# Performance work log

Hardware: AMD Instinct MI355X
Metric: run time of the kernel (lower is better)

## Reference

```python
import jax, jax.numpy as jnp
import numpy as np

DIM_MODEL = 1024
NUM_HEADS = 16
DIM_K = DIM_MODEL // NUM_HEADS
B, S = 4, 2048


def setup_inputs() -> dict:
    key = jax.random.key(0)
    ks = jax.random.split(key, 11)
    std = 1.0 / np.sqrt(DIM_MODEL)  # kaiming_normal fan_in, gain sqrt(2)/sqrt(fan_in); use simple scale
    kaiming = np.sqrt(2.0 / DIM_MODEL)
    return {
        "query": jax.random.normal(ks[0], (B, S, DIM_MODEL), dtype=jnp.float32),
        "key": jax.random.normal(ks[1], (B, S, DIM_MODEL), dtype=jnp.float32),
        "value": jax.random.normal(ks[2], (B, S, DIM_MODEL), dtype=jnp.float32),
        "W_q": jax.random.normal(ks[3], (DIM_MODEL, DIM_MODEL), dtype=jnp.float32) * kaiming,
        "b_q": jnp.zeros((DIM_MODEL,), dtype=jnp.float32),
        "W_k": jax.random.normal(ks[4], (DIM_MODEL, DIM_MODEL), dtype=jnp.float32) * kaiming,
        "b_k": jnp.zeros((DIM_MODEL,), dtype=jnp.float32),
        "W_v": jax.random.normal(ks[5], (DIM_MODEL, DIM_MODEL), dtype=jnp.float32) * kaiming,
        "b_v": jnp.zeros((DIM_MODEL,), dtype=jnp.float32),
        "W_o": jax.random.normal(ks[6], (DIM_MODEL, DIM_MODEL), dtype=jnp.float32) * kaiming,
        "b_o": jnp.zeros((DIM_MODEL,), dtype=jnp.float32),
    }


def _split_heads(x):
    b, s, _ = x.shape
    return x.reshape(b, s, NUM_HEADS, DIM_K).transpose(0, 2, 1, 3)  # [B,H,S,Dk]


def reference(query, key, value, W_q, b_q, W_k, b_k, W_v, b_v, W_o, b_o):
    # torch Linear: y = x @ W.T + b; dropout p=0.0 -> identity
    q = _split_heads(query @ W_q.T + b_q)
    k = _split_heads(key @ W_k.T + b_k)
    v = _split_heads(value @ W_v.T + b_v)
    scale = 1.0 / np.sqrt(DIM_K)
    scores = jnp.einsum("bhqd,bhkd->bhqk", q, k) * scale  # [B,H,S,S]
    probs = jax.nn.softmax(scores, axis=-1)
    attn = jnp.einsum("bhqk,bhkd->bhqd", probs, v)
    out = attn.transpose(0, 2, 1, 3).reshape(query.shape[0], query.shape[1], DIM_MODEL)
    return out @ W_o.T + b_o
```

## Files before the change

### kernel.cpp

```cpp
#include <hip/hip_runtime.h>
#include <stdint.h>

typedef __bf16 bf16x8 __attribute__((ext_vector_type(8)));
typedef __bf16 bf16x4 __attribute__((ext_vector_type(4)));
typedef float f32x4 __attribute__((ext_vector_type(4)));

static __device__ __forceinline__ unsigned short f2bf(float f) {
  unsigned u = __builtin_bit_cast(unsigned, f);
  u += 0x7fffu + ((u >> 16) & 1u);
  return (unsigned short)(u >> 16);
}

static __device__ __forceinline__ unsigned short bfu(float x) {
  __bf16 b = (__bf16)x;
  return __builtin_bit_cast(unsigned short, b);
}

#if __has_builtin(__builtin_amdgcn_exp2f)
#define EXP2(x) __builtin_amdgcn_exp2f(x)
#else
#define EXP2(x) __expf(0.69314718055994531f * (x))
#endif

static __device__ __forceinline__ void gload_lds16(const void* g, void* l) {
  __builtin_amdgcn_global_load_lds(
      (const __attribute__((address_space(1))) unsigned int*)(uintptr_t)g,
      (__attribute__((address_space(3))) unsigned int*)(uintptr_t)l, 16, 0, 0);
}

#define BIGU 2097152
#define WU   262144
__global__ __launch_bounds__(256) void cvt_all(const float* __restrict__ q,  const float* __restrict__ k,
                                               const float* __restrict__ v,  const float* __restrict__ wq,
                                               const float* __restrict__ wk, const float* __restrict__ wv,
                                               const float* __restrict__ wo, ushort4* __restrict__ dst) {
  int u = blockIdx.x * 256 + threadIdx.x;
  const float4* src;
  if (u < BIGU)            src = (const float4*)q + u;
  else if (u < 2 * BIGU)   src = (const float4*)k + (u - BIGU);
  else if (u < 3 * BIGU)   src = (const float4*)v + (u - 2 * BIGU);
  else {
    int r = u - 3 * BIGU;
    if (r < WU)            src = (const float4*)wq + r;
    else if (r < 2 * WU)   src = (const float4*)wk + (r - WU);
    else if (r < 3 * WU)   src = (const float4*)wv + (r - 2 * WU);
    else                   src = (const float4*)wo + (r - 3 * WU);
  }
  float4 f = *src;
  ushort4 o;
  o.x = f2bf(f.x); o.y = f2bf(f.y); o.z = f2bf(f.z); o.w = f2bf(f.w);
  dst[u] = o;
}

#define GM 8192
#define GN 1024
#define GK 1024

template <bool OUTF32, bool TRIPLE>
__global__ __launch_bounds__(256, 2) void gemm_bt(const unsigned short* __restrict__ A0,
                                                  const unsigned short* __restrict__ W0,
                                                  const float* __restrict__ bias0,
                                                  const float* __restrict__ bias1,
                                                  const float* __restrict__ bias2,
                                                  void* __restrict__ Cout) {
  __shared__ unsigned short As[2][128 * 64];
  __shared__ unsigned short Bs[2][128 * 64];
  const int z = TRIPLE ? blockIdx.z : 0;
  const unsigned short* A  = A0 + (size_t)z * ((size_t)GM * GK);
  const unsigned short* Bw = W0 + (size_t)z * ((size_t)GN * GK);
  const float* bias = TRIPLE ? (z == 0 ? bias0 : (z == 1 ? bias1 : bias2)) : bias0;

  const int tid = threadIdx.x;
  const int w = tid >> 6;
  const int lane = tid & 63;
  const int lq = lane & 15;
  const int g = lane >> 4;
  const int bm = blockIdx.y * 128;
  const int bn = blockIdx.x * 128;
  const int srow = lane >> 3;
  const int schunk = (lane & 7) ^ srow;
  const int wrow = (w >> 1) * 64;
  const int wcol = (w & 1) * 64;

  f32x4 acc[4][4] = {};

#define STAGE(ktv, bufv)                                                                   \
  do {                                                                                     \
    _Pragma("unroll") for (int j = 0; j < 4; ++j) {                                        \
      const int r0 = w * 32 + j * 8;                                                       \
      gload_lds16(A  + (size_t)(bm + r0 + srow) * GK + (ktv) * 64 + schunk * 8,            \
                  &As[bufv][r0 * 64]);                                                     \
      gload_lds16(Bw + (size_t)(bn + r0 + srow) * GK + (ktv) * 64 + schunk * 8,            \
                  &Bs[bufv][r0 * 64]);                                                     \
    }                                                                                      \
  } while (0)

  STAGE(0, 0);
  __syncthreads();

  for (int kt = 0; kt < GK / 64; ++kt) {
    const int cur = kt & 1;
    if (kt < GK / 64 - 1) STAGE(kt + 1, cur ^ 1);

#pragma unroll
    for (int kk = 0; kk < 2; ++kk) {
      bf16x8 af[4], bfv[4];
#pragma unroll
      for (int mt = 0; mt < 4; ++mt) {
        int m = wrow + mt * 16 + lq;
        af[mt] = *(const bf16x8*)&As[cur][m * 64 + ((kk * 32 + g * 8) ^ ((m & 7) << 3))];
      }
#pragma unroll
      for (int nt = 0; nt < 4; ++nt) {
        int n = wcol + nt * 16 + lq;
        bfv[nt] = *(const bf16x8*)&Bs[cur][n * 64 + ((kk * 32 + g * 8) ^ ((n & 7) << 3))];
      }
#pragma unroll
      for (int mt = 0; mt < 4; ++mt)
#pragma unroll
        for (int nt = 0; nt < 4; ++nt)
          acc[mt][nt] = __builtin_amdgcn_mfma_f32_16x16x32_bf16(af[mt], bfv[nt], acc[mt][nt], 0, 0, 0);
    }
    __syncthreads();
  }
#undef STAGE

  float bvs[4];
#pragma unroll
  for (int nt = 0; nt < 4; ++nt) bvs[nt] = bias[bn + wcol + nt * 16 + lq];

#pragma unroll
  for (int mt = 0; mt < 4; ++mt) {
#pragma unroll
    for (int nt = 0; nt < 4; ++nt) {
#pragma unroll
      for (int r = 0; r < 4; ++r) {
        int m = bm + wrow + mt * 16 + g * 4 + r;
        int n = bn + wcol + nt * 16 + lq;
        float v = acc[mt][nt][r] + bvs[nt];
        if (OUTF32) ((float*)Cout)[(size_t)m * GN + n] = v;
        else ((unsigned short*)Cout)[(size_t)z * ((size_t)GM * GN) + (size_t)m * GN + n] = f2bf(v);
      }
    }
  }
}

#define TRRD(dst, off) \
  asm volatile("ds_read_b64_tr_b16 %0, %1 offset:" off \
               : "=v"(dst) \
               : "v"((const __attribute__((address_space(3))) unsigned short*)(uintptr_t)vb))

__global__ __launch_bounds__(256, 3) void attn_fwd(const unsigned short* __restrict__ Qp,
                                                   const unsigned short* __restrict__ Kp,
                                                   const unsigned short* __restrict__ Vp,
                                                   unsigned short* __restrict__ Op) {
  __shared__ unsigned short Ks[2][4096];
  __shared__ unsigned short Vs[2][4096];
  __shared__ unsigned short Pl[8][1024];
  const int tid = threadIdx.x;
  const int w = tid >> 6;
  const int lane = tid & 63;
  const int lq = lane & 15;
  const int g = lane >> 4;
  const int qt = blockIdx.x;
  const int bh = blockIdx.y;
  const int b = bh >> 4;
  const int h = bh & 15;
  const size_t rowbase = (size_t)b * 2048;
  const int hcol = h * 64;

  const int c0 = w * 2, c1 = w * 2 + 1;
  const int srow = lane >> 3;
  const int schunk = (lane & 7) ^ srow;
  const int vkeyl = (lane >> 5) * 4 + ((lane >> 1) & 3);
  const int vd0   = ((lane >> 3) & 3) * 16 + (lane & 1) * 8;

  const unsigned short* kq = Kp + rowbase * 1024 + hcol;
  const unsigned short* vq = Vp + rowbase * 1024 + hcol;

  bf16x8 qf[2][2];
#pragma unroll
  for (int qh = 0; qh < 2; ++qh) {
    const int qrow = qt * 128 + w * 32 + qh * 16 + lq;
#pragma unroll
    for (int kk = 0; kk < 2; ++kk)
      qf[qh][kk] = *(const bf16x8*)&Qp[(rowbase + qrow) * 1024 + hcol + kk * 32 + g * 8];
  }

  const float ks2 = 0.125f * 1.44269504088896f;
  float m0 = -1e30f, m1 = -1e30f, l0 = 0.f, l1 = 0.f;
  f32x4 oa[2][4] = {};
  unsigned short* Pw0 = Pl[w * 2];
  unsigned short* Pw1 = Pl[w * 2 + 1];
  const int pxor = (lq & 7) << 3;
  const int kxor = pxor;

  {
    gload_lds16(kq + (size_t)(c0 * 8 + srow) * 1024 + schunk * 8, &Ks[0][c0 * 512]);
    gload_lds16(kq + (size_t)(c1 * 8 + srow) * 1024 + schunk * 8, &Ks[0][c1 * 512]);
    gload_lds16(vq + (size_t)(c0 * 8 + vkeyl) * 1024 + vd0, &Vs[0][c0 * 512]);
    gload_lds16(vq + (size_t)(c1 * 8 + vkeyl) * 1024 + vd0, &Vs[0][c1 * 512]);
  }
  __syncthreads();

  for (int j = 0; j < 32; ++j) {
    const int cur = j & 1;
    if (j < 31) {
      const size_t so = (size_t)(j + 1) * 64 * 1024;
      gload_lds16(kq + so + (size_t)(c0 * 8 + srow) * 1024 + schunk * 8, &Ks[cur ^ 1][c0 * 512]);
      gload_lds16(kq + so + (size_t)(c1 * 8 + srow) * 1024 + schunk * 8, &Ks[cur ^ 1][c1 * 512]);
      gload_lds16(vq + so + (size_t)(c0 * 8 + vkeyl) * 1024 + vd0, &Vs[cur ^ 1][c0 * 512]);
      gload_lds16(vq + so + (size_t)(c1 * 8 + vkeyl) * 1024 + vd0, &Vs[cur ^ 1][c1 * 512]);
    }

    f32x4 cc[2][4];
#pragma unroll
    for (int qh = 0; qh < 2; ++qh)
#pragma unroll
      for (int t = 0; t < 4; ++t) cc[qh][t] = (f32x4){0.f, 0.f, 0.f, 0.f};
#pragma unroll
    for (int t = 0; t < 4; ++t) {
      const int rb = (t * 16 + lq) * 64;
#pragma unroll
      for (int kk = 0; kk < 2; ++kk) {
        bf16x8 kf = *(const bf16x8*)&Ks[cur][rb + ((kk * 32 + g * 8) ^ kxor)];
        cc[0][t] = __builtin_amdgcn_mfma_f32_16x16x32_bf16(kf, qf[0][kk], cc[0][t], 0, 0, 0);
        cc[1][t] = __builtin_amdgcn_mfma_f32_16x16x32_bf16(kf, qf[1][kk], cc[1][t], 0, 0, 0);
      }
    }

    float t0 = cc[0][0][0], t1 = cc[1][0][0];
#pragma unroll
    for (int t = 0; t < 4; ++t)
#pragma unroll
      for (int r = 0; r < 4; ++r) {
        t0 = fmaxf(t0, cc[0][t][r]);
        t1 = fmaxf(t1, cc[1][t][r]);
      }
    t0 = fmaxf(t0, __shfl_xor(t0, 16)); t0 = fmaxf(t0, __shfl_xor(t0, 32));
    t1 = fmaxf(t1, __shfl_xor(t1, 16)); t1 = fmaxf(t1, __shfl_xor(t1, 32));

    const int defer = (t0 - m0 <= 64.f) && (t1 - m1 <= 64.f);
    if (!__all(defer)) {
      float n0 = fmaxf(m0, t0), n1 = fmaxf(m1, t1);
      float cr0 = EXP2(ks2 * (m0 - n0)), cr1 = EXP2(ks2 * (m1 - n1));
      l0 *= cr0; l1 *= cr1;
#pragma unroll
      for (int dt = 0; dt < 4; ++dt) { oa[0][dt] *= cr0; oa[1][dt] *= cr1; }
      m0 = n0; m1 = n1;
    }
    const float mk0 = m0 * ks2, mk1 = m1 * ks2;
    float ps0 = 0.f, ps1 = 0.f;
#pragma unroll
    for (int t = 0; t < 4; ++t) {
      float a0 = EXP2(__builtin_fmaf(cc[0][t][0], ks2, -mk0));
      float a1 = EXP2(__builtin_fmaf(cc[0][t][1], ks2, -mk0));
      float a2 = EXP2(__builtin_fmaf(cc[0][t][2], ks2, -mk0));
      float a3 = EXP2(__builtin_fmaf(cc[0][t][3], ks2, -mk0));
      ps0 += (a0 + a1) + (a2 + a3);
      ushort4 pk0; pk0.x = bfu(a0); pk0.y = bfu(a1); pk0.z = bfu(a2); pk0.w = bfu(a3);
      *(ushort4*)&Pw0[lq * 64 + ((t * 16 + g * 4) ^ pxor)] = pk0;
      float b0 = EXP2(__builtin_fmaf(cc[1][t][0], ks2, -mk1));
      float b1 = EXP2(__builtin_fmaf(cc[1][t][1], ks2, -mk1));
      float b2 = EXP2(__builtin_fmaf(cc[1][t][2], ks2, -mk1));
      float b3 = EXP2(__builtin_fmaf(cc[1][t][3], ks2, -mk1));
      ps1 += (b0 + b1) + (b2 + b3);
      ushort4 pk1; pk1.x = bfu(b0); pk1.y = bfu(b1); pk1.z = bfu(b2); pk1.w = bfu(b3);
      *(ushort4*)&Pw1[lq * 64 + ((t * 16 + g * 4) ^ pxor)] = pk1;
    }
    l0 += ps0; l1 += ps1;

    bf16x8 pf[2][2];
#pragma unroll
    for (int qh = 0; qh < 2; ++qh) {
      unsigned short* Pw = qh ? Pw1 : Pw0;
#pragma unroll
      for (int kk = 0; kk < 2; ++kk)
        pf[qh][kk] = *(const bf16x8*)&Pw[lq * 64 + ((kk * 32 + g * 8) ^ pxor)];
    }
    const unsigned short* vb =
        &Vs[cur][g * 512 + ((lane >> 2) & 3) * 16 + (lane & 3) * 4];
    bf16x4 T[16];
    TRRD(T[0],  "0");    TRRD(T[1],  "128");  TRRD(T[2],  "256");  TRRD(T[3],  "384");
    TRRD(T[4],  "512");  TRRD(T[5],  "640");  TRRD(T[6],  "768");  TRRD(T[7],  "896");
    TRRD(T[8],  "4096"); TRRD(T[9],  "4224"); TRRD(T[10], "4352"); TRRD(T[11], "4480");
    TRRD(T[12], "4608"); TRRD(T[13], "4736"); TRRD(T[14], "4864"); TRRD(T[15], "4992");
    asm volatile("s_waitcnt lgkmcnt(0)" ::: "memory");
    __builtin_amdgcn_sched_barrier(0);
#pragma unroll
    for (int kk = 0; kk < 2; ++kk) {
#pragma unroll
      for (int dt = 0; dt < 4; ++dt) {
        bf16x8 vf = __builtin_shufflevector(T[kk * 8 + dt], T[kk * 8 + 4 + dt],
                                            0, 1, 2, 3, 4, 5, 6, 7);
        oa[0][dt] = __builtin_amdgcn_mfma_f32_16x16x32_bf16(vf, pf[0][kk], oa[0][dt], 0, 0, 0);
        oa[1][dt] = __builtin_amdgcn_mfma_f32_16x16x32_bf16(vf, pf[1][kk], oa[1][dt], 0, 0, 0);
      }
    }
    __syncthreads();
  }

  l0 += __shfl_xor(l0, 16); l0 += __shfl_xor(l0, 32);
  l1 += __shfl_xor(l1, 16); l1 += __shfl_xor(l1, 32);
  float inv0 = 1.0f / l0, inv1 = 1.0f / l1;
#pragma unroll
  for (int qh = 0; qh < 2; ++qh) {
    const float inv = qh ? inv1 : inv0;
    const int qrow = qt * 128 + w * 32 + qh * 16 + lq;
#pragma unroll
    for (int dt = 0; dt < 4; ++dt) {
      ushort4 pk;
      pk.x = bfu(oa[qh][dt][0] * inv);
      pk.y = bfu(oa[qh][dt][1] * inv);
      pk.z = bfu(oa[qh][dt][2] * inv);
      pk.w = bfu(oa[qh][dt][3] * inv);
      *(ushort4*)&Op[(rowbase + qrow) * 1024 + hcol + dt * 16 + g * 4] = pk;
    }
  }
}

extern "C" void kernel_launch(void* const* d_in, const int* in_sizes, int n_in,
                              void* d_out, int out_size, void* d_ws, size_t ws_size,
                              hipStream_t stream) {
  const float* q  = (const float*)d_in[0];
  const float* k  = (const float*)d_in[1];
  const float* v  = (const float*)d_in[2];
  const float* Wq = (const float*)d_in[3];
  const float* bq = (const float*)d_in[4];
  const float* Wk = (const float*)d_in[5];
  const float* bk = (const float*)d_in[6];
  const float* Wv = (const float*)d_in[7];
  const float* bv = (const float*)d_in[8];
  const float* Wo = (const float*)d_in[9];
  const float* bo = (const float*)d_in[10];

  unsigned short* ws = (unsigned short*)d_ws;
  const size_t SZ  = (size_t)8192 * 1024;
  const size_t WSZ = (size_t)1024 * 1024;
  unsigned short* Xq  = ws;
  unsigned short* Wqb = Xq + 3 * SZ;
  unsigned short* Qp  = Wqb + 4 * WSZ;
  unsigned short* Kp  = Qp + SZ;
  unsigned short* Vp  = Kp + SZ;
  unsigned short* Wob = Wqb + 3 * WSZ;
  unsigned short* At  = Xq;

  cvt_all<<<(3 * BIGU + 4 * WU) / 256, 256, 0, stream>>>(q, k, v, Wq, Wk, Wv, Wo, (ushort4*)ws);

  gemm_bt<false, true><<<dim3(GN / 128, GM / 128, 3), 256, 0, stream>>>(Xq, Wqb, bq, bk, bv, Qp);

  attn_fwd<<<dim3(16, 64), 256, 0, stream>>>(Qp, Kp, Vp, At);

  gemm_bt<true, false><<<dim3(GN / 128, GM / 128, 1), 256, 0, stream>>>(At, Wob, bo, bo, bo, (float*)d_out);
}
```

Before: 353.8 us.

## Double query rows per attention block and raise MFMA wave priority

```diff
diff --git a/kernel.cpp b/kernel.cpp
--- a/kernel.cpp
+++ b/kernel.cpp
@@ -150,13 +150,13 @@
                : "=v"(dst) \
                : "v"((const __attribute__((address_space(3))) unsigned short*)(uintptr_t)vb))
 
-__global__ __launch_bounds__(256, 3) void attn_fwd(const unsigned short* __restrict__ Qp,
+__global__ __launch_bounds__(256, 2) void attn_fwd(const unsigned short* __restrict__ Qp,
                                                    const unsigned short* __restrict__ Kp,
                                                    const unsigned short* __restrict__ Vp,
                                                    unsigned short* __restrict__ Op) {
   __shared__ unsigned short Ks[2][4096];
   __shared__ unsigned short Vs[2][4096];
-  __shared__ unsigned short Pl[8][1024];
+  __shared__ unsigned short Pl[16][1024];
   const int tid = threadIdx.x;
   const int w = tid >> 6;
   const int lane = tid & 63;
@@ -178,29 +178,26 @@
   const unsigned short* kq = Kp + rowbase * 1024 + hcol;
   const unsigned short* vq = Vp + rowbase * 1024 + hcol;
 
-  bf16x8 qf[2][2];
-#pragma unroll
-  for (int qh = 0; qh < 2; ++qh) {
-    const int qrow = qt * 128 + w * 32 + qh * 16 + lq;
+  bf16x8 qf[4][2];
+#pragma unroll
+  for (int qh = 0; qh < 4; ++qh) {
+    const int qrow = qt * 256 + w * 64 + qh * 16 + lq;
 #pragma unroll
     for (int kk = 0; kk < 2; ++kk)
       qf[qh][kk] = *(const bf16x8*)&Qp[(rowbase + qrow) * 1024 + hcol + kk * 32 + g * 8];
   }
 
   const float ks2 = 0.125f * 1.44269504088896f;
-  float m0 = -1e30f, m1 = -1e30f, l0 = 0.f, l1 = 0.f;
-  f32x4 oa[2][4] = {};
-  unsigned short* Pw0 = Pl[w * 2];
-  unsigned short* Pw1 = Pl[w * 2 + 1];
+  float mr[4] = {-1e30f, -1e30f, -1e30f, -1e30f};
+  float lr[4] = {0.f, 0.f, 0.f, 0.f};
+  f32x4 oa[4][4] = {};
   const int pxor = (lq & 7) << 3;
   const int kxor = pxor;
 
-  {
-    gload_lds16(kq + (size_t)(c0 * 8 + srow) * 1024 + schunk * 8, &Ks[0][c0 * 512]);
-    gload_lds16(kq + (size_t)(c1 * 8 + srow) * 1024 + schunk * 8, &Ks[0][c1 * 512]);
-    gload_lds16(vq + (size_t)(c0 * 8 + vkeyl) * 1024 + vd0, &Vs[0][c0 * 512]);
-    gload_lds16(vq + (size_t)(c1 * 8 + vkeyl) * 1024 + vd0, &Vs[0][c1 * 512]);
-  }
+  gload_lds16(kq + (size_t)(c0 * 8 + srow) * 1024 + schunk * 8, &Ks[0][c0 * 512]);
+  gload_lds16(kq + (size_t)(c1 * 8 + srow) * 1024 + schunk * 8, &Ks[0][c1 * 512]);
+  gload_lds16(vq + (size_t)(c0 * 8 + vkeyl) * 1024 + vd0, &Vs[0][c0 * 512]);
+  gload_lds16(vq + (size_t)(c1 * 8 + vkeyl) * 1024 + vd0, &Vs[0][c1 * 512]);
   __syncthreads();
 
   for (int j = 0; j < 32; ++j) {
@@ -213,67 +210,74 @@
       gload_lds16(vq + so + (size_t)(c1 * 8 + vkeyl) * 1024 + vd0, &Vs[cur ^ 1][c1 * 512]);
     }
 
-    f32x4 cc[2][4];
-#pragma unroll
-    for (int qh = 0; qh < 2; ++qh)
+    f32x4 cc[4][4];
+#pragma unroll
+    for (int qh = 0; qh < 4; ++qh)
 #pragma unroll
       for (int t = 0; t < 4; ++t) cc[qh][t] = (f32x4){0.f, 0.f, 0.f, 0.f};
+    __builtin_amdgcn_s_setprio(1);
 #pragma unroll
     for (int t = 0; t < 4; ++t) {
       const int rb = (t * 16 + lq) * 64;
 #pragma unroll
       for (int kk = 0; kk < 2; ++kk) {
         bf16x8 kf = *(const bf16x8*)&Ks[cur][rb + ((kk * 32 + g * 8) ^ kxor)];
-        cc[0][t] = __builtin_amdgcn_mfma_f32_16x16x32_bf16(kf, qf[0][kk], cc[0][t], 0, 0, 0);
-        cc[1][t] = __builtin_amdgcn_mfma_f32_16x16x32_bf16(kf, qf[1][kk], cc[1][t], 0, 0, 0);
-      }
-    }
-
-    float t0 = cc[0][0][0], t1 = cc[1][0][0];
-#pragma unroll
-    for (int t = 0; t < 4; ++t)
-#pragma unroll
-      for (int r = 0; r < 4; ++r) {
-        t0 = fmaxf(t0, cc[0][t][r]);
-        t1 = fmaxf(t1, cc[1][t][r]);
-      }
-    t0 = fmaxf(t0, __shfl_xor(t0, 16)); t0 = fmaxf(t0, __shfl_xor(t0, 32));
-    t1 = fmaxf(t1, __shfl_xor(t1, 16)); t1 = fmaxf(t1, __shfl_xor(t1, 32));
-
-    const int defer = (t0 - m0 <= 64.f) && (t1 - m1 <= 64.f);
+#pragma unroll
+        for (int qh = 0; qh < 4; ++qh)
+          cc[qh][t] = __builtin_amdgcn_mfma_f32_16x16x32_bf16(kf, qf[qh][kk], cc[qh][t], 0, 0, 0);
+      }
+    }
+    __builtin_amdgcn_s_setprio(0);
+
+    float tm[4];
+#pragma unroll
+    for (int qh = 0; qh < 4; ++qh) {
+      float t0 = cc[qh][0][0];
+#pragma unroll
+      for (int t = 0; t < 4; ++t)
+#pragma unroll
+        for (int r = 0; r < 4; ++r) t0 = fmaxf(t0, cc[qh][t][r]);
+      t0 = fmaxf(t0, __shfl_xor(t0, 16));
+      t0 = fmaxf(t0, __shfl_xor(t0, 32));
+      tm[qh] = t0;
+    }
+    int defer = 1;
+#pragma unroll
+    for (int qh = 0; qh < 4; ++qh) defer &= (tm[qh] - mr[qh] <= 64.f);
     if (!__all(defer)) {
-      float n0 = fmaxf(m0, t0), n1 = fmaxf(m1, t1);
-      float cr0 = EXP2(ks2 * (m0 - n0)), cr1 = EXP2(ks2 * (m1 - n1));
-      l0 *= cr0; l1 *= cr1;
-#pragma unroll
-      for (int dt = 0; dt < 4; ++dt) { oa[0][dt] *= cr0; oa[1][dt] *= cr1; }
-      m0 = n0; m1 = n1;
-    }
-    const float mk0 = m0 * ks2, mk1 = m1 * ks2;
-    float ps0 = 0.f, ps1 = 0.f;
-#pragma unroll
-    for (int t = 0; t < 4; ++t) {
-      float a0 = EXP2(__builtin_fmaf(cc[0][t][0], ks2, -mk0));
-      float a1 = EXP2(__builtin_fmaf(cc[0][t][1], ks2, -mk0));
-      float a2 = EXP2(__builtin_fmaf(cc[0][t][2], ks2, -mk0));
-      float a3 = EXP2(__builtin_fmaf(cc[0][t][3], ks2, -mk0));
-      ps0 += (a0 + a1) + (a2 + a3);
-      ushort4 pk0; pk0.x = bfu(a0); pk0.y = bfu(a1); pk0.z = bfu(a2); pk0.w = bfu(a3);
-      *(ushort4*)&Pw0[lq * 64 + ((t * 16 + g * 4) ^ pxor)] = pk0;
-      float b0 = EXP2(__builtin_fmaf(cc[1][t][0], ks2, -mk1));
-      float b1 = EXP2(__builtin_fmaf(cc[1][t][1], ks2, -mk1));
-      float b2 = EXP2(__builtin_fmaf(cc[1][t][2], ks2, -mk1));
-      float b3 = EXP2(__builtin_fmaf(cc[1][t][3], ks2, -mk1));
-      ps1 += (b0 + b1) + (b2 + b3);
-      ushort4 pk1; pk1.x = bfu(b0); pk1.y = bfu(b1); pk1.z = bfu(b2); pk1.w = bfu(b3);
-      *(ushort4*)&Pw1[lq * 64 + ((t * 16 + g * 4) ^ pxor)] = pk1;
-    }
-    l0 += ps0; l1 += ps1;
-
-    bf16x8 pf[2][2];
-#pragma unroll
-    for (int qh = 0; qh < 2; ++qh) {
-      unsigned short* Pw = qh ? Pw1 : Pw0;
+#pragma unroll
+      for (int qh = 0; qh < 4; ++qh) {
+        float n = fmaxf(mr[qh], tm[qh]);
+        float cr = EXP2(ks2 * (mr[qh] - n));
+        lr[qh] *= cr;
+#pragma unroll
+        for (int dt = 0; dt < 4; ++dt) oa[qh][dt] *= cr;
+        mr[qh] = n;
+      }
+    }
+#pragma unroll
+    for (int qh = 0; qh < 4; ++qh) {
+      const float mk = mr[qh] * ks2;
+      float ps = 0.f;
+      unsigned short* Pw = Pl[w * 4 + qh];
+#pragma unroll
+      for (int t = 0; t < 4; ++t) {
+        float a0 = EXP2(__builtin_fmaf(cc[qh][t][0], ks2, -mk));
+        float a1 = EXP2(__builtin_fmaf(cc[qh][t][1], ks2, -mk));
+        float a2 = EXP2(__builtin_fmaf(cc[qh][t][2], ks2, -mk));
+        float a3 = EXP2(__builtin_fmaf(cc[qh][t][3], ks2, -mk));
+        ps += (a0 + a1) + (a2 + a3);
+        ushort4 pk;
+        pk.x = bfu(a0); pk.y = bfu(a1); pk.z = bfu(a2); pk.w = bfu(a3);
+        *(ushort4*)&Pw[lq * 64 + ((t * 16 + g * 4) ^ pxor)] = pk;
+      }
+      lr[qh] += ps;
+    }
+
+    bf16x8 pf[4][2];
+#pragma unroll
+    for (int qh = 0; qh < 4; ++qh) {
+      unsigned short* Pw = Pl[w * 4 + qh];
 #pragma unroll
       for (int kk = 0; kk < 2; ++kk)
         pf[qh][kk] = *(const bf16x8*)&Pw[lq * 64 + ((kk * 32 + g * 8) ^ pxor)];
@@ -287,26 +291,29 @@
     TRRD(T[12], "4608"); TRRD(T[13], "4736"); TRRD(T[14], "4864"); TRRD(T[15], "4992");
     asm volatile("s_waitcnt lgkmcnt(0)" ::: "memory");
     __builtin_amdgcn_sched_barrier(0);
+    __builtin_amdgcn_s_setprio(1);
 #pragma unroll
     for (int kk = 0; kk < 2; ++kk) {
 #pragma unroll
       for (int dt = 0; dt < 4; ++dt) {
         bf16x8 vf = __builtin_shufflevector(T[kk * 8 + dt], T[kk * 8 + 4 + dt],
                                             0, 1, 2, 3, 4, 5, 6, 7);
-        oa[0][dt] = __builtin_amdgcn_mfma_f32_16x16x32_bf16(vf, pf[0][kk], oa[0][dt], 0, 0, 0);
-        oa[1][dt] = __builtin_amdgcn_mfma_f32_16x16x32_bf16(vf, pf[1][kk], oa[1][dt], 0, 0, 0);
-      }
-    }
+#pragma unroll
+        for (int qh = 0; qh < 4; ++qh)
+          oa[qh][dt] = __builtin_amdgcn_mfma_f32_16x16x32_bf16(vf, pf[qh][kk], oa[qh][dt], 0, 0, 0);
+      }
+    }
+    __builtin_amdgcn_s_setprio(0);
     __syncthreads();
   }
 
-  l0 += __shfl_xor(l0, 16); l0 += __shfl_xor(l0, 32);
-  l1 += __shfl_xor(l1, 16); l1 += __shfl_xor(l1, 32);
-  float inv0 = 1.0f / l0, inv1 = 1.0f / l1;
-#pragma unroll
-  for (int qh = 0; qh < 2; ++qh) {
-    const float inv = qh ? inv1 : inv0;
-    const int qrow = qt * 128 + w * 32 + qh * 16 + lq;
+#pragma unroll
+  for (int qh = 0; qh < 4; ++qh) {
+    float l = lr[qh];
+    l += __shfl_xor(l, 16);
+    l += __shfl_xor(l, 32);
+    const float inv = 1.0f / l;
+    const int qrow = qt * 256 + w * 64 + qh * 16 + lq;
 #pragma unroll
     for (int dt = 0; dt < 4; ++dt) {
       ushort4 pk;
@@ -349,7 +356,7 @@
 
   gemm_bt<false, true><<<dim3(GN / 128, GM / 128, 3), 256, 0, stream>>>(Xq, Wqb, bq, bk, bv, Qp);
 
-  attn_fwd<<<dim3(16, 64), 256, 0, stream>>>(Qp, Kp, Vp, At);
+  attn_fwd<<<dim3(8, 64), 256, 0, stream>>>(Qp, Kp, Vp, At);
 
   gemm_bt<true, false><<<dim3(GN / 128, GM / 128, 1), 256, 0, stream>>>(At, Wob, bo, bo, bo, (float*)d_out);
 }
```

Result: faster. 341.5 us (-3.5%).

## Switch attention to 32x32x16 MFMA and keep P in registers via permlane swap

Applied to the files above, without the earlier changes.

```diff
diff --git a/kernel.cpp b/kernel.cpp
--- a/kernel.cpp
+++ b/kernel.cpp
@@ -4,6 +4,7 @@
 typedef __bf16 bf16x8 __attribute__((ext_vector_type(8)));
 typedef __bf16 bf16x4 __attribute__((ext_vector_type(4)));
 typedef float f32x4 __attribute__((ext_vector_type(4)));
+typedef float f32x16 __attribute__((ext_vector_type(16)));
 
 static __device__ __forceinline__ unsigned short f2bf(float f) {
   unsigned u = __builtin_bit_cast(unsigned, f);
@@ -14,6 +15,27 @@
 static __device__ __forceinline__ unsigned short bfu(float x) {
   __bf16 b = (__bf16)x;
   return __builtin_bit_cast(unsigned short, b);
+}
+
+static __device__ __forceinline__ unsigned cvtpk(float lo, float hi) {
+  unsigned r;
+  asm("v_cvt_pk_bf16_f32 %0, %1, %2" : "=v"(r) : "v"(lo), "v"(hi));
+  return r;
+}
+
+static __device__ __forceinline__ void plswap(unsigned a, unsigned b,
+                                              unsigned& x, unsigned& y) {
+#if __has_builtin(__builtin_amdgcn_permlane32_swap)
+  auto r = __builtin_amdgcn_permlane32_swap((int)a, (int)b, false, false);
+  x = (unsigned)r[0];
+  y = (unsigned)r[1];
+#else
+  unsigned ap = (unsigned)__shfl_xor((int)a, 32);
+  unsigned bp = (unsigned)__shfl_xor((int)b, 32);
+  const bool lo = (threadIdx.x & 32) == 0;
+  x = lo ? a : bp;
+  y = lo ? ap : b;
+#endif
 }
 
 #if __has_builtin(__builtin_amdgcn_exp2f)
@@ -150,18 +172,17 @@
                : "=v"(dst) \
                : "v"((const __attribute__((address_space(3))) unsigned short*)(uintptr_t)vb))
 
-__global__ __launch_bounds__(256, 3) void attn_fwd(const unsigned short* __restrict__ Qp,
+__global__ __launch_bounds__(256, 4) void attn_fwd(const unsigned short* __restrict__ Qp,
                                                    const unsigned short* __restrict__ Kp,
                                                    const unsigned short* __restrict__ Vp,
                                                    unsigned short* __restrict__ Op) {
   __shared__ unsigned short Ks[2][4096];
   __shared__ unsigned short Vs[2][4096];
-  __shared__ unsigned short Pl[8][1024];
   const int tid = threadIdx.x;
   const int w = tid >> 6;
   const int lane = tid & 63;
-  const int lq = lane & 15;
-  const int g = lane >> 4;
+  const int q32 = lane & 31;
+  const int l5 = lane >> 5;
   const int qt = blockIdx.x;
   const int bh = blockIdx.y;
   const int b = bh >> 4;
@@ -178,29 +199,27 @@
   const unsigned short* kq = Kp + rowbase * 1024 + hcol;
   const unsigned short* vq = Vp + rowbase * 1024 + hcol;
 
-  bf16x8 qf[2][2];
-#pragma unroll
-  for (int qh = 0; qh < 2; ++qh) {
-    const int qrow = qt * 128 + w * 32 + qh * 16 + lq;
-#pragma unroll
-    for (int kk = 0; kk < 2; ++kk)
-      qf[qh][kk] = *(const bf16x8*)&Qp[(rowbase + qrow) * 1024 + hcol + kk * 32 + g * 8];
-  }
+  const int qrow = qt * 128 + w * 32 + q32;
+  bf16x8 qf[4];
+#pragma unroll
+  for (int ks = 0; ks < 4; ++ks)
+    qf[ks] = *(const bf16x8*)&Qp[(rowbase + qrow) * 1024 + hcol + ks * 16 + l5 * 8];
 
   const float ks2 = 0.125f * 1.44269504088896f;
-  float m0 = -1e30f, m1 = -1e30f, l0 = 0.f, l1 = 0.f;
-  f32x4 oa[2][4] = {};
-  unsigned short* Pw0 = Pl[w * 2];
-  unsigned short* Pw1 = Pl[w * 2 + 1];
-  const int pxor = (lq & 7) << 3;
-  const int kxor = pxor;
-
-  {
-    gload_lds16(kq + (size_t)(c0 * 8 + srow) * 1024 + schunk * 8, &Ks[0][c0 * 512]);
-    gload_lds16(kq + (size_t)(c1 * 8 + srow) * 1024 + schunk * 8, &Ks[0][c1 * 512]);
-    gload_lds16(vq + (size_t)(c0 * 8 + vkeyl) * 1024 + vd0, &Vs[0][c0 * 512]);
-    gload_lds16(vq + (size_t)(c1 * 8 + vkeyl) * 1024 + vd0, &Vs[0][c1 * 512]);
-  }
+  float mreg = -1e30f, lsum = 0.f;
+  f32x16 oa[2] = {};
+
+  const int rbase = q32 * 64;
+  const int kxor = (lane & 7) << 3;
+  int coff[4];
+#pragma unroll
+  for (int ks = 0; ks < 4; ++ks) coff[ks] = (ks * 16 + l5 * 8) ^ kxor;
+  const int vboff = l5 * 512 + ((lane >> 4) & 1) * 64 + ((lane >> 2) & 3) * 16 + (lane & 3) * 4;
+
+  gload_lds16(kq + (size_t)(c0 * 8 + srow) * 1024 + schunk * 8, &Ks[0][c0 * 512]);
+  gload_lds16(kq + (size_t)(c1 * 8 + srow) * 1024 + schunk * 8, &Ks[0][c1 * 512]);
+  gload_lds16(vq + (size_t)(c0 * 8 + vkeyl) * 1024 + vd0, &Vs[0][c0 * 512]);
+  gload_lds16(vq + (size_t)(c1 * 8 + vkeyl) * 1024 + vd0, &Vs[0][c1 * 512]);
   __syncthreads();
 
   for (int j = 0; j < 32; ++j) {
@@ -213,108 +232,88 @@
       gload_lds16(vq + so + (size_t)(c1 * 8 + vkeyl) * 1024 + vd0, &Vs[cur ^ 1][c1 * 512]);
     }
 
-    f32x4 cc[2][4];
-#pragma unroll
-    for (int qh = 0; qh < 2; ++qh)
-#pragma unroll
-      for (int t = 0; t < 4; ++t) cc[qh][t] = (f32x4){0.f, 0.f, 0.f, 0.f};
-#pragma unroll
-    for (int t = 0; t < 4; ++t) {
-      const int rb = (t * 16 + lq) * 64;
-#pragma unroll
-      for (int kk = 0; kk < 2; ++kk) {
-        bf16x8 kf = *(const bf16x8*)&Ks[cur][rb + ((kk * 32 + g * 8) ^ kxor)];
-        cc[0][t] = __builtin_amdgcn_mfma_f32_16x16x32_bf16(kf, qf[0][kk], cc[0][t], 0, 0, 0);
-        cc[1][t] = __builtin_amdgcn_mfma_f32_16x16x32_bf16(kf, qf[1][kk], cc[1][t], 0, 0, 0);
-      }
-    }
-
-    float t0 = cc[0][0][0], t1 = cc[1][0][0];
-#pragma unroll
-    for (int t = 0; t < 4; ++t)
-#pragma unroll
-      for (int r = 0; r < 4; ++r) {
-        t0 = fmaxf(t0, cc[0][t][r]);
-        t1 = fmaxf(t1, cc[1][t][r]);
-      }
-    t0 = fmaxf(t0, __shfl_xor(t0, 16)); t0 = fmaxf(t0, __shfl_xor(t0, 32));
-    t1 = fmaxf(t1, __shfl_xor(t1, 16)); t1 = fmaxf(t1, __shfl_xor(t1, 32));
-
-    const int defer = (t0 - m0 <= 64.f) && (t1 - m1 <= 64.f);
-    if (!__all(defer)) {
-      float n0 = fmaxf(m0, t0), n1 = fmaxf(m1, t1);
-      float cr0 = EXP2(ks2 * (m0 - n0)), cr1 = EXP2(ks2 * (m1 - n1));
-      l0 *= cr0; l1 *= cr1;
-#pragma unroll
-      for (int dt = 0; dt < 4; ++dt) { oa[0][dt] *= cr0; oa[1][dt] *= cr1; }
-      m0 = n0; m1 = n1;
-    }
-    const float mk0 = m0 * ks2, mk1 = m1 * ks2;
-    float ps0 = 0.f, ps1 = 0.f;
-#pragma unroll
-    for (int t = 0; t < 4; ++t) {
-      float a0 = EXP2(__builtin_fmaf(cc[0][t][0], ks2, -mk0));
-      float a1 = EXP2(__builtin_fmaf(cc[0][t][1], ks2, -mk0));
-      float a2 = EXP2(__builtin_fmaf(cc[0][t][2], ks2, -mk0));
-      float a3 = EXP2(__builtin_fmaf(cc[0][t][3], ks2, -mk0));
-      ps0 += (a0 + a1) + (a2 + a3);
-      ushort4 pk0; pk0.x = bfu(a0); pk0.y = bfu(a1); pk0.z = bfu(a2); pk0.w = bfu(a3);
-      *(ushort4*)&Pw0[lq * 64 + ((t * 16 + g * 4) ^ pxor)] = pk0;
-      float b0 = EXP2(__builtin_fmaf(cc[1][t][0], ks2, -mk1));
-      float b1 = EXP2(__builtin_fmaf(cc[1][t][1], ks2, -mk1));
-      float b2 = EXP2(__builtin_fmaf(cc[1][t][2], ks2, -mk1));
-      float b3 = EXP2(__builtin_fmaf(cc[1][t][3], ks2, -mk1));
-      ps1 += (b0 + b1) + (b2 + b3);
-      ushort4 pk1; pk1.x = bfu(b0); pk1.y = bfu(b1); pk1.z = bfu(b2); pk1.w = bfu(b3);
-      *(ushort4*)&Pw1[lq * 64 + ((t * 16 + g * 4) ^ pxor)] = pk1;
-    }
-    l0 += ps0; l1 += ps1;
-
-    bf16x8 pf[2][2];
-#pragma unroll
-    for (int qh = 0; qh < 2; ++qh) {
-      unsigned short* Pw = qh ? Pw1 : Pw0;
-#pragma unroll
-      for (int kk = 0; kk < 2; ++kk)
-        pf[qh][kk] = *(const bf16x8*)&Pw[lq * 64 + ((kk * 32 + g * 8) ^ pxor)];
-    }
-    const unsigned short* vb =
-        &Vs[cur][g * 512 + ((lane >> 2) & 3) * 16 + (lane & 3) * 4];
-    bf16x4 T[16];
-    TRRD(T[0],  "0");    TRRD(T[1],  "128");  TRRD(T[2],  "256");  TRRD(T[3],  "384");
-    TRRD(T[4],  "512");  TRRD(T[5],  "640");  TRRD(T[6],  "768");  TRRD(T[7],  "896");
-    TRRD(T[8],  "4096"); TRRD(T[9],  "4224"); TRRD(T[10], "4352"); TRRD(T[11], "4480");
-    TRRD(T[12], "4608"); TRRD(T[13], "4736"); TRRD(T[14], "4864"); TRRD(T[15], "4992");
-    asm volatile("s_waitcnt lgkmcnt(0)" ::: "memory");
-    __builtin_amdgcn_sched_barrier(0);
-#pragma unroll
-    for (int kk = 0; kk < 2; ++kk) {
-#pragma unroll
-      for (int dt = 0; dt < 4; ++dt) {
-        bf16x8 vf = __builtin_shufflevector(T[kk * 8 + dt], T[kk * 8 + 4 + dt],
-                                            0, 1, 2, 3, 4, 5, 6, 7);
-        oa[0][dt] = __builtin_amdgcn_mfma_f32_16x16x32_bf16(vf, pf[0][kk], oa[0][dt], 0, 0, 0);
-        oa[1][dt] = __builtin_amdgcn_mfma_f32_16x16x32_bf16(vf, pf[1][kk], oa[1][dt], 0, 0, 0);
-      }
+#pragma unroll
+    for (int kt = 0; kt < 2; ++kt) {
+      f32x16 c = {};
+      __builtin_amdgcn_s_setprio(1);
+#pragma unroll
+      for (int ks = 0; ks < 4; ++ks) {
+        bf16x8 kf = *(const bf16x8*)&Ks[cur][kt * 2048 + rbase + coff[ks]];
+        c = __builtin_amdgcn_mfma_f32_32x32x16_bf16(kf, qf[ks], c, 0, 0, 0);
+      }
+      __builtin_amdgcn_s_setprio(0);
+
+      const unsigned short* vb = &Vs[cur][kt * 2048 + vboff];
+      bf16x4 T[8];
+      TRRD(T[0], "0");    TRRD(T[1], "512");
+      TRRD(T[2], "256");  TRRD(T[3], "768");
+      TRRD(T[4], "2048"); TRRD(T[5], "2560");
+      TRRD(T[6], "2304"); TRRD(T[7], "2816");
+
+      float a0 = fmaxf(c[0], c[1]),   a1 = fmaxf(c[2], c[3]);
+      float a2 = fmaxf(c[4], c[5]),   a3 = fmaxf(c[6], c[7]);
+      float a4 = fmaxf(c[8], c[9]),   a5 = fmaxf(c[10], c[11]);
+      float a6 = fmaxf(c[12], c[13]), a7 = fmaxf(c[14], c[15]);
+      a0 = fmaxf(a0, a1); a2 = fmaxf(a2, a3); a4 = fmaxf(a4, a5); a6 = fmaxf(a6, a7);
+      a0 = fmaxf(a0, a2); a4 = fmaxf(a4, a6);
+      float tm = fmaxf(a0, a4);
+      tm = fmaxf(tm, __shfl_xor(tm, 32));
+
+      if (!__all(tm - mreg <= 64.f)) {
+        float n = fmaxf(mreg, tm);
+        float cr = EXP2(ks2 * (mreg - n));
+        lsum *= cr;
+        oa[0] *= cr; oa[1] *= cr;
+        mreg = n;
+      }
+      const float mk = mreg * ks2;
+      float p[16];
+#pragma unroll
+      for (int r = 0; r < 16; ++r) p[r] = EXP2(__builtin_fmaf(c[r], ks2, -mk));
+      float s0 = (p[0] + p[1]) + (p[2] + p[3]);
+      float s1 = (p[4] + p[5]) + (p[6] + p[7]);
+      float s2 = (p[8] + p[9]) + (p[10] + p[11]);
+      float s3 = (p[12] + p[13]) + (p[14] + p[15]);
+      lsum += (s0 + s1) + (s2 + s3);
+
+      asm volatile("s_waitcnt lgkmcnt(0)" ::: "memory");
+      __builtin_amdgcn_sched_barrier(0);
+
+      __builtin_amdgcn_s_setprio(1);
+#pragma unroll
+      for (int t2 = 0; t2 < 2; ++t2) {
+        unsigned pA0 = cvtpk(p[8 * t2 + 0], p[8 * t2 + 1]);
+        unsigned pA1 = cvtpk(p[8 * t2 + 2], p[8 * t2 + 3]);
+        unsigned pB0 = cvtpk(p[8 * t2 + 4], p[8 * t2 + 5]);
+        unsigned pB1 = cvtpk(p[8 * t2 + 6], p[8 * t2 + 7]);
+        unsigned w0, w1, w2, w3;
+        plswap(pA0, pB0, w0, w2);
+        plswap(pA1, pB1, w1, w3);
+        uint4 wv; wv.x = w0; wv.y = w1; wv.z = w2; wv.w = w3;
+        bf16x8 pf = __builtin_bit_cast(bf16x8, wv);
+        bf16x8 vf0 = __builtin_shufflevector(T[t2 * 4 + 0], T[t2 * 4 + 1], 0, 1, 2, 3, 4, 5, 6, 7);
+        oa[0] = __builtin_amdgcn_mfma_f32_32x32x16_bf16(vf0, pf, oa[0], 0, 0, 0);
+        bf16x8 vf1 = __builtin_shufflevector(T[t2 * 4 + 2], T[t2 * 4 + 3], 0, 1, 2, 3, 4, 5, 6, 7);
+        oa[1] = __builtin_amdgcn_mfma_f32_32x32x16_bf16(vf1, pf, oa[1], 0, 0, 0);
+      }
+      __builtin_amdgcn_s_setprio(0);
     }
     __syncthreads();
   }
 
-  l0 += __shfl_xor(l0, 16); l0 += __shfl_xor(l0, 32);
-  l1 += __shfl_xor(l1, 16); l1 += __shfl_xor(l1, 32);
-  float inv0 = 1.0f / l0, inv1 = 1.0f / l1;
-#pragma unroll
-  for (int qh = 0; qh < 2; ++qh) {
-    const float inv = qh ? inv1 : inv0;
-    const int qrow = qt * 128 + w * 32 + qh * 16 + lq;
-#pragma unroll
-    for (int dt = 0; dt < 4; ++dt) {
+  lsum += __shfl_xor(lsum, 32);
+  const float inv = 1.0f / lsum;
+#pragma unroll
+  for (int dt = 0; dt < 2; ++dt) {
+#pragma unroll
+    for (int jj = 0; jj < 4; ++jj) {
       ushort4 pk;
-      pk.x = bfu(oa[qh][dt][0] * inv);
-      pk.y = bfu(oa[qh][dt][1] * inv);
-      pk.z = bfu(oa[qh][dt][2] * inv);
-      pk.w = bfu(oa[qh][dt][3] * inv);
-      *(ushort4*)&Op[(rowbase + qrow) * 1024 + hcol + dt * 16 + g * 4] = pk;
+      pk.x = bfu(oa[dt][4 * jj + 0] * inv);
+      pk.y = bfu(oa[dt][4 * jj + 1] * inv);
+      pk.z = bfu(oa[dt][4 * jj + 2] * inv);
+      pk.w = bfu(oa[dt][4 * jj + 3] * inv);
+      const int d0 = dt * 32 + 8 * jj + 4 * l5;
+      *(ushort4*)&Op[(rowbase + qrow) * 1024 + hcol + d0] = pk;
     }
   }
 }
```

Result: no change. 349.4 us (-1.3%).
